# Performance work log

Hardware: AMD Instinct MI355X
Metric: run time of the kernel (lower is better)

The kernel has to match this reference:

```python
import jax, jax.numpy as jnp
import numpy as np

DIM = 2048
N_HEADS = 32
N_KV_HEADS = 8
HEAD_DIM = DIM // N_HEADS  # 64
GROUP = N_HEADS // N_KV_HEADS  # 4
ROPE_BASE = 10000.0


def setup_inputs() -> dict:
    key = jax.random.key(0)
    k1, k2, k3, k4, k5 = jax.random.split(key, 5)
    b, s = 1, 2048
    scale = 1.0 / np.sqrt(DIM)
    return {
        "x": jax.random.normal(k1, (b, s, DIM), dtype=jnp.float32),
        # weights stored as (in, out); equivalent math to torch Linear (x @ W.T)
        "wq": jax.random.normal(k2, (DIM, N_HEADS * HEAD_DIM), dtype=jnp.float32) * scale,
        "wk": jax.random.normal(k3, (DIM, N_KV_HEADS * HEAD_DIM), dtype=jnp.float32) * scale,
        "wv": jax.random.normal(k4, (DIM, N_KV_HEADS * HEAD_DIM), dtype=jnp.float32) * scale,
        "wo": jax.random.normal(k5, (N_HEADS * HEAD_DIM, DIM), dtype=jnp.float32) * scale,
    }


def _rope_cos_sin(seq_len, dtype):
    inv_freq = 1.0 / (ROPE_BASE ** (jnp.arange(0, HEAD_DIM, 2, dtype=jnp.float32) / HEAD_DIM))
    t = jnp.arange(seq_len, dtype=jnp.float32)
    freqs = jnp.outer(t, inv_freq)              # [s, hd/2]
    emb = jnp.concatenate([freqs, freqs], -1)   # [s, hd]
    return jnp.cos(emb).astype(dtype), jnp.sin(emb).astype(dtype)


def _rotate_half(x):
    x1, x2 = x[..., : HEAD_DIM // 2], x[..., HEAD_DIM // 2 :]
    return jnp.concatenate([-x2, x1], axis=-1)


def reference(x, wq, wk, wv, wo):
    b, s, _ = x.shape
    q = (x @ wq).reshape(b, s, N_HEADS, HEAD_DIM)
    k = (x @ wk).reshape(b, s, N_KV_HEADS, HEAD_DIM)
    v = (x @ wv).reshape(b, s, N_KV_HEADS, HEAD_DIM)

    cos, sin = _rope_cos_sin(s, x.dtype)
    cos = cos[None, :, None, :]  # [1, s, 1, hd] broadcast over batch & heads
    sin = sin[None, :, None, :]
    q = q * cos + _rotate_half(q) * sin
    k = k * cos + _rotate_half(k) * sin

    # GQA: repeat KV heads (repeat_interleave along head dim)
    k = jnp.repeat(k, GROUP, axis=2)  # [b, s, n_heads, hd]
    v = jnp.repeat(v, GROUP, axis=2)

    q = q.transpose(0, 2, 1, 3)  # [b, h, s, d]
    k = k.transpose(0, 2, 1, 3)
    v = v.transpose(0, 2, 1, 3)

    scores = jnp.einsum("bhqd,bhkd->bhqk", q, k) / jnp.sqrt(jnp.asarray(HEAD_DIM, x.dtype))
    attn = jax.nn.softmax(scores, axis=-1)
    out = jnp.einsum("bhqk,bhkd->bhqd", attn, v)
    out = out.transpose(0, 2, 1, 3).reshape(b, s, N_HEADS * HEAD_DIM)
    return out @ wo
```

## Files before the change

kernel.cpp:

```cpp
#include <hip/hip_runtime.h>
#include <hip/hip_bf16.h>

typedef __bf16 bf16x8 __attribute__((ext_vector_type(8)));
typedef __bf16 bf16x4 __attribute__((ext_vector_type(4)));
typedef float fx4 __attribute__((ext_vector_type(4)));
typedef float fx16 __attribute__((ext_vector_type(16)));

#define AS1 __attribute__((address_space(1)))
#define AS3 __attribute__((address_space(3)))

__global__ __launch_bounds__(256) void cast_x(const float4* __restrict__ X, __bf16* __restrict__ Xb) {
    int i = blockIdx.x * 256 + threadIdx.x;
    float4 v = X[i];
    bf16x4 o = { (__bf16)v.x, (__bf16)v.y, (__bf16)v.z, (__bf16)v.w };
    *(bf16x4*)(Xb + (size_t)i * 4) = o;
}

__global__ __launch_bounds__(256) void transpose_all(const float* __restrict__ wq, const float* __restrict__ wk,
                                                     const float* __restrict__ wv, const float* __restrict__ wo,
                                                     __bf16* __restrict__ WqkvT, __bf16* __restrict__ WoT) {
    constexpr int K = 2048;
    __shared__ float t[32][33];
    const int bx = blockIdx.x;
    const float* W; __bf16* Wt; int N, n0;
    if (bx < 64)      { W = wq; Wt = WqkvT;                        N = 2048; n0 = bx * 32; }
    else if (bx < 80) { W = wk; Wt = WqkvT + (size_t)2048 * 2048;  N = 512;  n0 = (bx - 64) * 32; }
    else if (bx < 96) { W = wv; Wt = WqkvT + (size_t)2560 * 2048;  N = 512;  n0 = (bx - 80) * 32; }
    else              { W = wo; Wt = WoT;                          N = 2048; n0 = (bx - 96) * 32; }
    const int tx = threadIdx.x & 31, ty = threadIdx.x >> 5;
    const int k0 = blockIdx.y * 32;
#pragma unroll
    for (int i = 0; i < 4; ++i)
        t[ty + i * 8][tx] = W[(size_t)(k0 + ty + i * 8) * N + n0 + tx];
    __syncthreads();
#pragma unroll
    for (int i = 0; i < 4; ++i)
        Wt[(size_t)(n0 + ty + i * 8) * K + k0 + tx] = (__bf16)t[tx][ty + i * 8];
}

__global__ __launch_bounds__(256) void gemm_qkv(const __bf16* __restrict__ A, const __bf16* __restrict__ Bt,
                                                __bf16* __restrict__ Qr, __bf16* __restrict__ Kr,
                                                __bf16* __restrict__ Vt) {
    constexpr int K = 2048;
    __shared__ __align__(16) __bf16 lA[2][128 * 32];
    __shared__ __align__(16) __bf16 lB[2][64 * 32];
    const int tid = threadIdx.x;
    const int wave = tid >> 6, lane = tid & 63;
    const int quad = lane >> 4, l16 = lane & 15;
    const int m0 = blockIdx.x * 128, n0 = blockIdx.y * 64;
    fx4 acc[2][4] = {};

    const __bf16* csrc[6]; __bf16* cdst[6];
#pragma unroll
    for (int it = 0; it < 6; ++it) {
        const int idx = wave * 6 + it;
        const int r4 = lane >> 2, c8 = (lane & 3) * 8;
        if (idx < 16) {
            const int kh = idx & 1, s = idx >> 1;
            csrc[it] = A + (size_t)(m0 + s * 16 + r4) * K + kh * 32 + c8;
            cdst[it] = &lA[kh][s * 512 + lane * 8];
        } else {
            const int b = idx - 16, kh = b & 1, s = b >> 1;
            csrc[it] = Bt + (size_t)(n0 + s * 16 + r4) * K + kh * 32 + c8;
            cdst[it] = &lB[kh][s * 512 + lane * 8];
        }
    }

    for (int k0 = 0; k0 < K; k0 += 64) {
        __syncthreads();
#pragma unroll
        for (int it = 0; it < 6; ++it)
            __builtin_amdgcn_global_load_lds((const AS1 void*)(csrc[it] + k0),
                                             (AS3 void*)cdst[it], 16, 0, 0);
        __builtin_amdgcn_s_waitcnt(0);
        __syncthreads();

#pragma unroll
        for (int kc = 0; kc < 2; ++kc) {
            bf16x8 af[2], bfr[4];
#pragma unroll
            for (int i = 0; i < 2; ++i) af[i] = *(const bf16x8*)&lA[kc][(wave * 32 + i * 16 + l16) * 32 + quad * 8];
#pragma unroll
            for (int j = 0; j < 4; ++j) bfr[j] = *(const bf16x8*)&lB[kc][(j * 16 + l16) * 32 + quad * 8];
#pragma unroll
            for (int i = 0; i < 2; ++i)
#pragma unroll
                for (int j = 0; j < 4; ++j)
                    acc[i][j] = __builtin_amdgcn_mfma_f32_16x16x32_bf16(af[i], bfr[j], acc[i][j], 0, 0, 0);
        }
    }

    const int by = blockIdx.y;
    if (by < 40) {
        const float scale = (by < 32) ? 0.18033688011112042f : 1.0f;
        __bf16* base = (by < 32) ? (Qr + (size_t)by * 2048 * 64)
                                 : (Kr + (size_t)(by - 32) * 2048 * 64);
#pragma unroll
        for (int jj = 0; jj < 2; ++jj) {
            const int dlo = jj * 16 + l16;
            const float inv = __builtin_amdgcn_exp2f(-(float)dlo * 0.41524101186092029f);
#pragma unroll
            for (int i = 0; i < 2; ++i)
#pragma unroll
                for (int r = 0; r < 4; ++r) {
                    const int s = m0 + wave * 32 + i * 16 + quad * 4 + r;
                    float sn, cs;
                    __sincosf((float)s * inv, &sn, &cs);
                    const float lo = acc[i][jj][r], hv = acc[i][jj + 2][r];
                    base[(size_t)s * 64 + dlo]      = (__bf16)((lo * cs - hv * sn) * scale);
                    base[(size_t)s * 64 + dlo + 32] = (__bf16)((hv * cs + lo * sn) * scale);
                }
        }
    } else {
        __bf16* vb = Vt + (size_t)(by - 40) * 64 * 2048;
#pragma unroll
        for (int i = 0; i < 2; ++i)
#pragma unroll
            for (int j = 0; j < 4; ++j) {
                const int d = j * 16 + l16;
                const int s0 = m0 + wave * 32 + i * 16 + quad * 4;
                bf16x4 p;
#pragma unroll
                for (int r = 0; r < 4; ++r) p[r] = (__bf16)acc[i][j][r];
                *(bf16x4*)&vb[(size_t)d * 2048 + s0] = p;
            }
    }
}

__global__ __launch_bounds__(256) void gemm_bt_sk(const __bf16* __restrict__ A, const __bf16* __restrict__ Bt,
                                                  float* __restrict__ C0, float* __restrict__ C1,
                                                  int M, int N, int K) {
    __shared__ __align__(16) __bf16 lA[128 * 32];
    __shared__ __align__(16) __bf16 lB[128 * 32];
    const int tid = threadIdx.x;
    const int wave = tid >> 6, lane = tid & 63;
    const int quad = lane >> 4, l16 = lane & 15;
    const int m0 = blockIdx.x * 128, n0 = blockIdx.y * 128;
    const int kz = blockIdx.z;
    const int kbeg = kz * (K >> 1), kend = kbeg + (K >> 1);
    float* C = kz ? C1 : C0;
    const int wm = (wave >> 1) * 64, wn = (wave & 1) * 64;
    fx4 acc[4][4] = {};

    const int st0 = wave * 1024;
    const int st1 = 4096 + wave * 1024;
    const int r0 = (st0 + lane * 16) >> 6, c0 = ((st0 + lane * 16) & 63) >> 1;
    const int r1 = (st1 + lane * 16) >> 6, c1 = ((st1 + lane * 16) & 63) >> 1;

    for (int k0 = kbeg; k0 < kend; k0 += 32) {
        __syncthreads();
        __builtin_amdgcn_global_load_lds((const AS1 void*)(A + (size_t)(m0 + r0) * K + k0 + c0),
                                         (AS3 void*)(lA + (st0 >> 1)), 16, 0, 0);
        __builtin_amdgcn_global_load_lds((const AS1 void*)(A + (size_t)(m0 + r1) * K + k0 + c1),
                                         (AS3 void*)(lA + (st1 >> 1)), 16, 0, 0);
        __builtin_amdgcn_global_load_lds((const AS1 void*)(Bt + (size_t)(n0 + r0) * K + k0 + c0),
                                         (AS3 void*)(lB + (st0 >> 1)), 16, 0, 0);
        __builtin_amdgcn_global_load_lds((const AS1 void*)(Bt + (size_t)(n0 + r1) * K + k0 + c1),
                                         (AS3 void*)(lB + (st1 >> 1)), 16, 0, 0);
        __builtin_amdgcn_s_waitcnt(0);
        __syncthreads();

        bf16x8 af[4], bfr[4];
#pragma unroll
        for (int i = 0; i < 4; ++i) af[i] = *(const bf16x8*)&lA[(wm + i * 16 + l16) * 32 + quad * 8];
#pragma unroll
        for (int j = 0; j < 4; ++j) bfr[j] = *(const bf16x8*)&lB[(wn + j * 16 + l16) * 32 + quad * 8];
#pragma unroll
        for (int i = 0; i < 4; ++i)
#pragma unroll
            for (int j = 0; j < 4; ++j)
                acc[i][j] = __builtin_amdgcn_mfma_f32_16x16x32_bf16(af[i], bfr[j], acc[i][j], 0, 0, 0);
    }
#pragma unroll
    for (int i = 0; i < 4; ++i)
#pragma unroll
        for (int j = 0; j < 4; ++j) {
            const int row = m0 + wm + i * 16 + quad * 4;
            const int col = n0 + wn + j * 16 + l16;
#pragma unroll
            for (int r = 0; r < 4; ++r)
                C[(size_t)(row + r) * N + col] = acc[i][j][r];
        }
}

__global__ __launch_bounds__(256) void reduce_add(float4* __restrict__ out, const float4* __restrict__ p) {
    const int i = blockIdx.x * 256 + threadIdx.x;
    float4 a = out[i];
    const float4 b = p[i];
    a.x += b.x; a.y += b.y; a.z += b.z; a.w += b.w;
    out[i] = a;
}

__global__ __launch_bounds__(256, 4) void flash_attn(const __bf16* __restrict__ Qr, const __bf16* __restrict__ Kr,
                                                     const __bf16* __restrict__ Vt, __bf16* __restrict__ O) {
    constexpr int S = 2048;
    __shared__ __align__(16) __bf16 lK[64 * 72];
    __shared__ __align__(16) __bf16 lV[64 * 72];
    const int qt = blockIdx.x, h = blockIdx.y, kvh = h >> 2;
    const int tid = threadIdx.x, wave = tid >> 6, lane = tid & 63;
    const int l32 = lane & 31, hi = lane >> 5;

    const int qrow = qt * 128 + wave * 32 + l32;
    const __bf16* qptr = Qr + ((size_t)h * S + qrow) * 64;
    bf16x8 qf[4];
#pragma unroll
    for (int kc = 0; kc < 4; ++kc) qf[kc] = *(const bf16x8*)(qptr + kc * 16 + hi * 8);

    const __bf16* Kbase = Kr + (size_t)kvh * S * 64;
    const __bf16* Vbase = Vt + (size_t)kvh * 64 * S;

    const int krow = tid >> 3;
    const int kcol = (tid & 7) * 8;
    const int vslot = (kcol & 48) | ((kcol & 8) >> 1);

    bf16x8 kreg0 = *(const bf16x8*)(Kbase + (size_t)krow * 64 + kcol);
    bf16x8 kreg1 = *(const bf16x8*)(Kbase + (size_t)(32 + krow) * 64 + kcol);
    bf16x8 vreg0 = *(const bf16x8*)(Vbase + (size_t)krow * S + kcol);
    bf16x8 vreg1 = *(const bf16x8*)(Vbase + (size_t)(32 + krow) * S + kcol);

    fx16 ov0, ov1;
#pragma unroll
    for (int i = 0; i < 16; ++i) { ov0[i] = 0.f; ov1[i] = 0.f; }
    float l_acc = 0.f;

    for (int kt = 0; kt < 32; ++kt) {
        __syncthreads();
        *(bf16x8*)&lK[krow * 72 + kcol] = kreg0;
        *(bf16x8*)&lK[(32 + krow) * 72 + kcol] = kreg1;
        bf16x4 v0lo = { vreg0[0], vreg0[1], vreg0[2], vreg0[3] };
        bf16x4 v0hi = { vreg0[4], vreg0[5], vreg0[6], vreg0[7] };
        bf16x4 v1lo = { vreg1[0], vreg1[1], vreg1[2], vreg1[3] };
        bf16x4 v1hi = { vreg1[4], vreg1[5], vreg1[6], vreg1[7] };
        *(bf16x4*)&lV[krow * 72 + vslot]            = v0lo;
        *(bf16x4*)&lV[krow * 72 + vslot + 8]        = v0hi;
        *(bf16x4*)&lV[(32 + krow) * 72 + vslot]     = v1lo;
        *(bf16x4*)&lV[(32 + krow) * 72 + vslot + 8] = v1hi;
        const int ktn = (kt + 1 < 32) ? kt + 1 : kt;
        kreg0 = *(const bf16x8*)(Kbase + (size_t)(ktn * 64 + krow) * 64 + kcol);
        kreg1 = *(const bf16x8*)(Kbase + (size_t)(ktn * 64 + 32 + krow) * 64 + kcol);
        vreg0 = *(const bf16x8*)(Vbase + (size_t)krow * S + ktn * 64 + kcol);
        vreg1 = *(const bf16x8*)(Vbase + (size_t)(32 + krow) * S + ktn * 64 + kcol);
        __syncthreads();

        fx16 sc0, sc1;
#pragma unroll
        for (int i = 0; i < 16; ++i) { sc0[i] = 0.f; sc1[i] = 0.f; }
#pragma unroll
        for (int kc = 0; kc < 4; ++kc) {
            const bf16x8 a0 = *(const bf16x8*)&lK[l32 * 72 + kc * 16 + hi * 8];
            const bf16x8 a1 = *(const bf16x8*)&lK[(32 + l32) * 72 + kc * 16 + hi * 8];
            sc0 = __builtin_amdgcn_mfma_f32_32x32x16_bf16(a0, qf[kc], sc0, 0, 0, 0);
            sc1 = __builtin_amdgcn_mfma_f32_32x32x16_bf16(a1, qf[kc], sc1, 0, 0, 0);
        }

#pragma unroll
        for (int h2 = 0; h2 < 2; ++h2) {
#pragma unroll
            for (int c = 0; c < 2; ++c) {
                bf16x8 pb;
#pragma unroll
                for (int j = 0; j < 8; ++j) {
                    const float sv = h2 ? sc1[c * 8 + j] : sc0[c * 8 + j];
                    const float p = __builtin_amdgcn_exp2f(sv);
                    l_acc += p;
                    pb[j] = (__bf16)p;
                }
                const int kcv = h2 * 2 + c;
                const bf16x8 va0 = *(const bf16x8*)&lV[l32 * 72 + kcv * 16 + hi * 8];
                const bf16x8 va1 = *(const bf16x8*)&lV[(32 + l32) * 72 + kcv * 16 + hi * 8];
                ov0 = __builtin_amdgcn_mfma_f32_32x32x16_bf16(va0, pb, ov0, 0, 0, 0);
                ov1 = __builtin_amdgcn_mfma_f32_32x32x16_bf16(va1, pb, ov1, 0, 0, 0);
            }
        }
    }

    const float l_tot = l_acc + __shfl_xor(l_acc, 32, 64);
    const float inv_l = 1.0f / l_tot;

#pragma unroll
    for (int dt = 0; dt < 2; ++dt)
#pragma unroll
        for (int rg2 = 0; rg2 < 4; ++rg2) {
            bf16x4 o4;
#pragma unroll
            for (int r = 0; r < 4; ++r)
                o4[r] = (__bf16)((dt ? ov1[rg2 * 4 + r] : ov0[rg2 * 4 + r]) * inv_l);
            const int col = h * 64 + dt * 32 + rg2 * 8 + hi * 4;
            *(bf16x4*)(O + (size_t)qrow * 2048 + col) = o4;
        }
}

extern "C" void kernel_launch(void* const* d_in, const int* in_sizes, int n_in,
                              void* d_out, int out_size, void* d_ws, size_t ws_size,
                              hipStream_t stream) {
    const float* x  = (const float*)d_in[0];
    const float* wq = (const float*)d_in[1];
    const float* wk = (const float*)d_in[2];
    const float* wv = (const float*)d_in[3];
    const float* wo = (const float*)d_in[4];
    float* out = (float*)d_out;
    char* ws = (char*)d_ws;

    __bf16* Xb    = (__bf16*)ws;
    __bf16* WqkvT = (__bf16*)(ws + ((size_t)8 << 20));
    __bf16* WoT   = (__bf16*)(ws + ((size_t)20 << 20));
    __bf16* Qr    = (__bf16*)(ws + ((size_t)28 << 20));
    __bf16* Kr    = (__bf16*)(ws + ((size_t)36 << 20));
    __bf16* Vt    = (__bf16*)(ws + ((size_t)38 << 20));
    __bf16* Ob    = (__bf16*)(ws + ((size_t)40 << 20));
    float*  Cp    = (float*)ws;

    cast_x<<<4096, 256, 0, stream>>>((const float4*)x, Xb);
    transpose_all<<<dim3(160, 64), 256, 0, stream>>>(wq, wk, wv, wo, WqkvT, WoT);

    gemm_qkv<<<dim3(16, 48), 256, 0, stream>>>(Xb, WqkvT, Qr, Kr, Vt);
    flash_attn<<<dim3(16, 32), 256, 0, stream>>>(Qr, Kr, Vt, Ob);
    gemm_bt_sk<<<dim3(16, 16, 2), 256, 0, stream>>>(Ob, WoT, out, Cp, 2048, 2048, 2048);
    reduce_add<<<4096, 256, 0, stream>>>((float4*)out, (const float4*)Cp);
}
```

Baseline: 228.0 us.

## Split attention KV loop across two wave groups with shared-memory reduction

The flash attention block grows from 256 to 512 threads. Two groups of four waves each handle alternating 64-key tiles for the same 128 query rows. Their unnormalized partial outputs and row sums are then combined through shared memory before normalization. This doubles the parallelism per query tile, since only 512 blocks were launched, and halves the serial KV loop length. The cost is extra LDS traffic, a final reduction step, and higher per-block resource use that may limit occupancy.

```diff
diff --git a/kernel.cpp b/kernel.cpp
--- a/kernel.cpp
+++ b/kernel.cpp
@@ -191,16 +191,19 @@
     out[i] = a;
 }
 
-__global__ __launch_bounds__(256, 4) void flash_attn(const __bf16* __restrict__ Qr, const __bf16* __restrict__ Kr,
+__global__ __launch_bounds__(512, 4) void flash_attn(const __bf16* __restrict__ Qr, const __bf16* __restrict__ Kr,
                                                      const __bf16* __restrict__ Vt, __bf16* __restrict__ O) {
     constexpr int S = 2048;
-    __shared__ __align__(16) __bf16 lK[64 * 72];
-    __shared__ __align__(16) __bf16 lV[64 * 72];
+    __shared__ __align__(16) __bf16 smem[4 * 64 * 72];
     const int qt = blockIdx.x, h = blockIdx.y, kvh = h >> 2;
     const int tid = threadIdx.x, wave = tid >> 6, lane = tid & 63;
+    const int grp = wave >> 2, w4 = wave & 3;
     const int l32 = lane & 31, hi = lane >> 5;
 
-    const int qrow = qt * 128 + wave * 32 + l32;
+    __bf16* lKg = smem + grp * 2 * 4608;
+    __bf16* lVg = lKg + 4608;
+
+    const int qrow = qt * 128 + w4 * 32 + l32;
     const __bf16* qptr = Qr + ((size_t)h * S + qrow) * 64;
     bf16x8 qf[4];
 #pragma unroll
@@ -209,33 +212,35 @@
     const __bf16* Kbase = Kr + (size_t)kvh * S * 64;
     const __bf16* Vbase = Vt + (size_t)kvh * 64 * S;
 
-    const int krow = tid >> 3;
-    const int kcol = (tid & 7) * 8;
+    const int gtid = tid & 255;
+    const int krow = gtid >> 3;
+    const int kcol = (gtid & 7) * 8;
     const int vslot = (kcol & 48) | ((kcol & 8) >> 1);
 
-    bf16x8 kreg0 = *(const bf16x8*)(Kbase + (size_t)krow * 64 + kcol);
-    bf16x8 kreg1 = *(const bf16x8*)(Kbase + (size_t)(32 + krow) * 64 + kcol);
-    bf16x8 vreg0 = *(const bf16x8*)(Vbase + (size_t)krow * S + kcol);
-    bf16x8 vreg1 = *(const bf16x8*)(Vbase + (size_t)(32 + krow) * S + kcol);
+    bf16x8 kreg0 = *(const bf16x8*)(Kbase + (size_t)(grp * 64 + krow) * 64 + kcol);
+    bf16x8 kreg1 = *(const bf16x8*)(Kbase + (size_t)(grp * 64 + 32 + krow) * 64 + kcol);
+    bf16x8 vreg0 = *(const bf16x8*)(Vbase + (size_t)krow * S + grp * 64 + kcol);
+    bf16x8 vreg1 = *(const bf16x8*)(Vbase + (size_t)(32 + krow) * S + grp * 64 + kcol);
 
     fx16 ov0, ov1;
 #pragma unroll
     for (int i = 0; i < 16; ++i) { ov0[i] = 0.f; ov1[i] = 0.f; }
     float l_acc = 0.f;
 
-    for (int kt = 0; kt < 32; ++kt) {
-        __syncthreads();
-        *(bf16x8*)&lK[krow * 72 + kcol] = kreg0;
-        *(bf16x8*)&lK[(32 + krow) * 72 + kcol] = kreg1;
+    for (int it = 0; it < 16; ++it) {
+        const int kt = it * 2 + grp;
+        __syncthreads();
+        *(bf16x8*)&lKg[krow * 72 + kcol] = kreg0;
+        *(bf16x8*)&lKg[(32 + krow) * 72 + kcol] = kreg1;
         bf16x4 v0lo = { vreg0[0], vreg0[1], vreg0[2], vreg0[3] };
         bf16x4 v0hi = { vreg0[4], vreg0[5], vreg0[6], vreg0[7] };
         bf16x4 v1lo = { vreg1[0], vreg1[1], vreg1[2], vreg1[3] };
         bf16x4 v1hi = { vreg1[4], vreg1[5], vreg1[6], vreg1[7] };
-        *(bf16x4*)&lV[krow * 72 + vslot]            = v0lo;
-        *(bf16x4*)&lV[krow * 72 + vslot + 8]        = v0hi;
-        *(bf16x4*)&lV[(32 + krow) * 72 + vslot]     = v1lo;
-        *(bf16x4*)&lV[(32 + krow) * 72 + vslot + 8] = v1hi;
-        const int ktn = (kt + 1 < 32) ? kt + 1 : kt;
+        *(bf16x4*)&lVg[krow * 72 + vslot]            = v0lo;
+        *(bf16x4*)&lVg[krow * 72 + vslot + 8]        = v0hi;
+        *(bf16x4*)&lVg[(32 + krow) * 72 + vslot]     = v1lo;
+        *(bf16x4*)&lVg[(32 + krow) * 72 + vslot + 8] = v1hi;
+        const int ktn = (it + 1 < 16) ? kt + 2 : kt;
         kreg0 = *(const bf16x8*)(Kbase + (size_t)(ktn * 64 + krow) * 64 + kcol);
         kreg1 = *(const bf16x8*)(Kbase + (size_t)(ktn * 64 + 32 + krow) * 64 + kcol);
         vreg0 = *(const bf16x8*)(Vbase + (size_t)krow * S + ktn * 64 + kcol);
@@ -247,8 +252,8 @@
         for (int i = 0; i < 16; ++i) { sc0[i] = 0.f; sc1[i] = 0.f; }
 #pragma unroll
         for (int kc = 0; kc < 4; ++kc) {
-            const bf16x8 a0 = *(const bf16x8*)&lK[l32 * 72 + kc * 16 + hi * 8];
-            const bf16x8 a1 = *(const bf16x8*)&lK[(32 + l32) * 72 + kc * 16 + hi * 8];
+            const bf16x8 a0 = *(const bf16x8*)&lKg[l32 * 72 + kc * 16 + hi * 8];
+            const bf16x8 a1 = *(const bf16x8*)&lKg[(32 + l32) * 72 + kc * 16 + hi * 8];
             sc0 = __builtin_amdgcn_mfma_f32_32x32x16_bf16(a0, qf[kc], sc0, 0, 0, 0);
             sc1 = __builtin_amdgcn_mfma_f32_32x32x16_bf16(a1, qf[kc], sc1, 0, 0, 0);
         }
@@ -266,28 +271,52 @@
                     pb[j] = (__bf16)p;
                 }
                 const int kcv = h2 * 2 + c;
-                const bf16x8 va0 = *(const bf16x8*)&lV[l32 * 72 + kcv * 16 + hi * 8];
-                const bf16x8 va1 = *(const bf16x8*)&lV[(32 + l32) * 72 + kcv * 16 + hi * 8];
+                const bf16x8 va0 = *(const bf16x8*)&lVg[l32 * 72 + kcv * 16 + hi * 8];
+                const bf16x8 va1 = *(const bf16x8*)&lVg[(32 + l32) * 72 + kcv * 16 + hi * 8];
                 ov0 = __builtin_amdgcn_mfma_f32_32x32x16_bf16(va0, pb, ov0, 0, 0, 0);
                 ov1 = __builtin_amdgcn_mfma_f32_32x32x16_bf16(va1, pb, ov1, 0, 0, 0);
             }
         }
     }
 
-    const float l_tot = l_acc + __shfl_xor(l_acc, 32, 64);
-    const float inv_l = 1.0f / l_tot;
-
-#pragma unroll
-    for (int dt = 0; dt < 2; ++dt)
-#pragma unroll
-        for (int rg2 = 0; rg2 < 4; ++rg2) {
-            bf16x4 o4;
-#pragma unroll
-            for (int r = 0; r < 4; ++r)
-                o4[r] = (__bf16)((dt ? ov1[rg2 * 4 + r] : ov0[rg2 * 4 + r]) * inv_l);
-            const int col = h * 64 + dt * 32 + rg2 * 8 + hi * 4;
-            *(bf16x4*)(O + (size_t)qrow * 2048 + col) = o4;
-        }
+    const float l_pair = l_acc + __shfl_xor(l_acc, 32, 64);
+
+    fx4* lO = (fx4*)smem;
+    float* lL = (float*)(smem + 16384);
+    __syncthreads();
+    if (grp == 1) {
+#pragma unroll
+        for (int ic = 0; ic < 4; ++ic) {
+            fx4 c0, c1;
+#pragma unroll
+            for (int r = 0; r < 4; ++r) { c0[r] = ov0[ic * 4 + r]; c1[r] = ov1[ic * 4 + r]; }
+            lO[(ic * 4 + w4) * 64 + lane] = c0;
+            lO[((ic + 4) * 4 + w4) * 64 + lane] = c1;
+        }
+        if (hi == 0) lL[w4 * 32 + l32] = l_pair;
+    }
+    __syncthreads();
+    if (grp == 0) {
+#pragma unroll
+        for (int ic = 0; ic < 4; ++ic) {
+            const fx4 c0 = lO[(ic * 4 + w4) * 64 + lane];
+            const fx4 c1 = lO[((ic + 4) * 4 + w4) * 64 + lane];
+#pragma unroll
+            for (int r = 0; r < 4; ++r) { ov0[ic * 4 + r] += c0[r]; ov1[ic * 4 + r] += c1[r]; }
+        }
+        const float inv_l = 1.0f / (l_pair + lL[w4 * 32 + l32]);
+#pragma unroll
+        for (int dt = 0; dt < 2; ++dt)
+#pragma unroll
+            for (int rg2 = 0; rg2 < 4; ++rg2) {
+                bf16x4 o4;
+#pragma unroll
+                for (int r = 0; r < 4; ++r)
+                    o4[r] = (__bf16)((dt ? ov1[rg2 * 4 + r] : ov0[rg2 * 4 + r]) * inv_l);
+                const int col = h * 64 + dt * 32 + rg2 * 8 + hi * 4;
+                *(bf16x4*)(O + (size_t)qrow * 2048 + col) = o4;
+            }
+    }
 }
 
 extern "C" void kernel_launch(void* const* d_in, const int* in_sizes, int n_in,
@@ -314,7 +343,7 @@
     transpose_all<<<dim3(160, 64), 256, 0, stream>>>(wq, wk, wv, wo, WqkvT, WoT);
 
     gemm_qkv<<<dim3(16, 48), 256, 0, stream>>>(Xb, WqkvT, Qr, Kr, Vt);
-    flash_attn<<<dim3(16, 32), 256, 0, stream>>>(Qr, Kr, Vt, Ob);
+    flash_attn<<<dim3(16, 32), 512, 0, stream>>>(Qr, Kr, Vt, Ob);
     gemm_bt_sk<<<dim3(16, 16, 2), 256, 0, stream>>>(Ob, WoT, out, Cp, 2048, 2048, 2048);
     reduce_add<<<4096, 256, 0, stream>>>((float4*)out, (const float4*)Cp);
 }
```

Result: faster. 222.8 us (-2.3%).

## Restructure flash attention into single-wave blocks without barriers over 32-key tiles

Applied to the files above, without the earlier changes.

The attention kernel moves from 256-thread blocks, where four waves share 64-key K/V tiles and synchronise twice per tile, to 64-thread single-wave blocks that each process 32 query rows over 32-key tiles. This removes the __syncthreads barriers and launches 2048 blocks instead of 512. Block ids are ordered so the eight KV heads vary fastest, which is meant to keep K/V reads hot in L2. In exchange each wave loads its own K/V tiles, so global and L2 traffic grows about fourfold, and each tile carries less MFMA work to hide load latency.

```diff
diff --git a/kernel.cpp b/kernel.cpp
--- a/kernel.cpp
+++ b/kernel.cpp
@@ -191,17 +191,20 @@
     out[i] = a;
 }
 
-__global__ __launch_bounds__(256, 4) void flash_attn(const __bf16* __restrict__ Qr, const __bf16* __restrict__ Kr,
-                                                     const __bf16* __restrict__ Vt, __bf16* __restrict__ O) {
+__global__ __launch_bounds__(64, 2) void flash_attn(const __bf16* __restrict__ Qr, const __bf16* __restrict__ Kr,
+                                                    const __bf16* __restrict__ Vt, __bf16* __restrict__ O) {
     constexpr int S = 2048;
-    __shared__ __align__(16) __bf16 lK[64 * 72];
+    __shared__ __align__(16) __bf16 lK[32 * 72];
     __shared__ __align__(16) __bf16 lV[64 * 72];
-    const int qt = blockIdx.x, h = blockIdx.y, kvh = h >> 2;
-    const int tid = threadIdx.x, wave = tid >> 6, lane = tid & 63;
+    const int id = blockIdx.x;
+    const int kvh = id & 7;
+    const int tq = id >> 3;
+    const int qtile = tq & 63;
+    const int h = kvh * 4 + (tq >> 6);
+    const int lane = threadIdx.x;
     const int l32 = lane & 31, hi = lane >> 5;
 
-    const int qrow = qt * 128 + wave * 32 + l32;
-    const __bf16* qptr = Qr + ((size_t)h * S + qrow) * 64;
+    const __bf16* qptr = Qr + ((size_t)h * S + qtile * 32 + l32) * 64;
     bf16x8 qf[4];
 #pragma unroll
     for (int kc = 0; kc < 4; ++kc) qf[kc] = *(const bf16x8*)(qptr + kc * 16 + hi * 8);
@@ -209,74 +212,84 @@
     const __bf16* Kbase = Kr + (size_t)kvh * S * 64;
     const __bf16* Vbase = Vt + (size_t)kvh * 64 * S;
 
-    const int krow = tid >> 3;
-    const int kcol = (tid & 7) * 8;
-    const int vslot = (kcol & 48) | ((kcol & 8) >> 1);
-
-    bf16x8 kreg0 = *(const bf16x8*)(Kbase + (size_t)krow * 64 + kcol);
-    bf16x8 kreg1 = *(const bf16x8*)(Kbase + (size_t)(32 + krow) * 64 + kcol);
-    bf16x8 vreg0 = *(const bf16x8*)(Vbase + (size_t)krow * S + kcol);
-    bf16x8 vreg1 = *(const bf16x8*)(Vbase + (size_t)(32 + krow) * S + kcol);
+    const int kr = lane >> 1, kc2 = (lane & 1) * 32;
+    const int vr = lane >> 2, vc = (lane & 3) * 8;
+    const int vslot = (vc & 16) | ((vc & 8) >> 1);
+
+    bf16x8 kst[4], vst[4];
+#pragma unroll
+    for (int u = 0; u < 4; ++u) kst[u] = *(const bf16x8*)(Kbase + (size_t)kr * 64 + kc2 + u * 8);
+#pragma unroll
+    for (int p = 0; p < 4; ++p) vst[p] = *(const bf16x8*)(Vbase + (size_t)(vr + p * 16) * S + vc);
+
+#pragma unroll
+    for (int u = 0; u < 4; ++u) *(bf16x8*)&lK[kr * 72 + kc2 + u * 8] = kst[u];
+#pragma unroll
+    for (int p = 0; p < 4; ++p) {
+        bf16x4 lo = { vst[p][0], vst[p][1], vst[p][2], vst[p][3] };
+        bf16x4 hi4 = { vst[p][4], vst[p][5], vst[p][6], vst[p][7] };
+        *(bf16x4*)&lV[(vr + p * 16) * 72 + vslot]     = lo;
+        *(bf16x4*)&lV[(vr + p * 16) * 72 + vslot + 8] = hi4;
+    }
+#pragma unroll
+    for (int u = 0; u < 4; ++u) kst[u] = *(const bf16x8*)(Kbase + (size_t)(32 + kr) * 64 + kc2 + u * 8);
+#pragma unroll
+    for (int p = 0; p < 4; ++p) vst[p] = *(const bf16x8*)(Vbase + (size_t)(vr + p * 16) * S + 32 + vc);
 
     fx16 ov0, ov1;
 #pragma unroll
     for (int i = 0; i < 16; ++i) { ov0[i] = 0.f; ov1[i] = 0.f; }
     float l_acc = 0.f;
 
-    for (int kt = 0; kt < 32; ++kt) {
-        __syncthreads();
-        *(bf16x8*)&lK[krow * 72 + kcol] = kreg0;
-        *(bf16x8*)&lK[(32 + krow) * 72 + kcol] = kreg1;
-        bf16x4 v0lo = { vreg0[0], vreg0[1], vreg0[2], vreg0[3] };
-        bf16x4 v0hi = { vreg0[4], vreg0[5], vreg0[6], vreg0[7] };
-        bf16x4 v1lo = { vreg1[0], vreg1[1], vreg1[2], vreg1[3] };
-        bf16x4 v1hi = { vreg1[4], vreg1[5], vreg1[6], vreg1[7] };
-        *(bf16x4*)&lV[krow * 72 + vslot]            = v0lo;
-        *(bf16x4*)&lV[krow * 72 + vslot + 8]        = v0hi;
-        *(bf16x4*)&lV[(32 + krow) * 72 + vslot]     = v1lo;
-        *(bf16x4*)&lV[(32 + krow) * 72 + vslot + 8] = v1hi;
-        const int ktn = (kt + 1 < 32) ? kt + 1 : kt;
-        kreg0 = *(const bf16x8*)(Kbase + (size_t)(ktn * 64 + krow) * 64 + kcol);
-        kreg1 = *(const bf16x8*)(Kbase + (size_t)(ktn * 64 + 32 + krow) * 64 + kcol);
-        vreg0 = *(const bf16x8*)(Vbase + (size_t)krow * S + ktn * 64 + kcol);
-        vreg1 = *(const bf16x8*)(Vbase + (size_t)(32 + krow) * S + ktn * 64 + kcol);
-        __syncthreads();
-
-        fx16 sc0, sc1;
-#pragma unroll
-        for (int i = 0; i < 16; ++i) { sc0[i] = 0.f; sc1[i] = 0.f; }
+    for (int it = 0; it < 64; ++it) {
+        fx16 sc;
+#pragma unroll
+        for (int i = 0; i < 16; ++i) sc[i] = 0.f;
 #pragma unroll
         for (int kc = 0; kc < 4; ++kc) {
-            const bf16x8 a0 = *(const bf16x8*)&lK[l32 * 72 + kc * 16 + hi * 8];
-            const bf16x8 a1 = *(const bf16x8*)&lK[(32 + l32) * 72 + kc * 16 + hi * 8];
-            sc0 = __builtin_amdgcn_mfma_f32_32x32x16_bf16(a0, qf[kc], sc0, 0, 0, 0);
-            sc1 = __builtin_amdgcn_mfma_f32_32x32x16_bf16(a1, qf[kc], sc1, 0, 0, 0);
-        }
-
-#pragma unroll
-        for (int h2 = 0; h2 < 2; ++h2) {
-#pragma unroll
-            for (int c = 0; c < 2; ++c) {
-                bf16x8 pb;
-#pragma unroll
-                for (int j = 0; j < 8; ++j) {
-                    const float sv = h2 ? sc1[c * 8 + j] : sc0[c * 8 + j];
-                    const float p = __builtin_amdgcn_exp2f(sv);
-                    l_acc += p;
-                    pb[j] = (__bf16)p;
-                }
-                const int kcv = h2 * 2 + c;
-                const bf16x8 va0 = *(const bf16x8*)&lV[l32 * 72 + kcv * 16 + hi * 8];
-                const bf16x8 va1 = *(const bf16x8*)&lV[(32 + l32) * 72 + kcv * 16 + hi * 8];
-                ov0 = __builtin_amdgcn_mfma_f32_32x32x16_bf16(va0, pb, ov0, 0, 0, 0);
-                ov1 = __builtin_amdgcn_mfma_f32_32x32x16_bf16(va1, pb, ov1, 0, 0, 0);
+            const bf16x8 a = *(const bf16x8*)&lK[l32 * 72 + kc * 16 + hi * 8];
+            sc = __builtin_amdgcn_mfma_f32_32x32x16_bf16(a, qf[kc], sc, 0, 0, 0);
+        }
+
+#pragma unroll
+        for (int c = 0; c < 2; ++c) {
+            bf16x8 pb;
+#pragma unroll
+            for (int j = 0; j < 8; ++j) {
+                const float p = __builtin_amdgcn_exp2f(sc[c * 8 + j]);
+                l_acc += p;
+                pb[j] = (__bf16)p;
             }
+            const bf16x8 va0 = *(const bf16x8*)&lV[l32 * 72 + c * 16 + hi * 8];
+            const bf16x8 va1 = *(const bf16x8*)&lV[(32 + l32) * 72 + c * 16 + hi * 8];
+            ov0 = __builtin_amdgcn_mfma_f32_32x32x16_bf16(va0, pb, ov0, 0, 0, 0);
+            ov1 = __builtin_amdgcn_mfma_f32_32x32x16_bf16(va1, pb, ov1, 0, 0, 0);
+        }
+
+        if (it + 1 < 64) {
+#pragma unroll
+            for (int u = 0; u < 4; ++u) *(bf16x8*)&lK[kr * 72 + kc2 + u * 8] = kst[u];
+#pragma unroll
+            for (int p = 0; p < 4; ++p) {
+                bf16x4 lo = { vst[p][0], vst[p][1], vst[p][2], vst[p][3] };
+                bf16x4 hi4 = { vst[p][4], vst[p][5], vst[p][6], vst[p][7] };
+                *(bf16x4*)&lV[(vr + p * 16) * 72 + vslot]     = lo;
+                *(bf16x4*)&lV[(vr + p * 16) * 72 + vslot + 8] = hi4;
+            }
+            const int ktn = (it + 2 < 64) ? it + 2 : 63;
+#pragma unroll
+            for (int u = 0; u < 4; ++u)
+                kst[u] = *(const bf16x8*)(Kbase + (size_t)(ktn * 32 + kr) * 64 + kc2 + u * 8);
+#pragma unroll
+            for (int p = 0; p < 4; ++p)
+                vst[p] = *(const bf16x8*)(Vbase + (size_t)(vr + p * 16) * S + ktn * 32 + vc);
         }
     }
 
     const float l_tot = l_acc + __shfl_xor(l_acc, 32, 64);
     const float inv_l = 1.0f / l_tot;
 
+    const int qrow = qtile * 32 + l32;
 #pragma unroll
     for (int dt = 0; dt < 2; ++dt)
 #pragma unroll
@@ -314,7 +327,7 @@
     transpose_all<<<dim3(160, 64), 256, 0, stream>>>(wq, wk, wv, wo, WqkvT, WoT);
 
     gemm_qkv<<<dim3(16, 48), 256, 0, stream>>>(Xb, WqkvT, Qr, Kr, Vt);
-    flash_attn<<<dim3(16, 32), 256, 0, stream>>>(Qr, Kr, Vt, Ob);
+    flash_attn<<<2048, 64, 0, stream>>>(Qr, Kr, Vt, Ob);
     gemm_bt_sk<<<dim3(16, 16, 2), 256, 0, stream>>>(Ob, WoT, out, Cp, 2048, 2048, 2048);
     reduce_add<<<4096, 256, 0, stream>>>((float4*)out, (const float4*)Cp);
 }
```

Result: slower. 245.3 us (+7.6%).
